# Kernel optimization log

Hardware: AMD Instinct MI355X
Metric: run time of the kernel (lower is better)

Reference implementation:

```python
import jax, jax.numpy as jnp
import numpy as np

VOCAB, EMB, HID = 32000, 32, 256
B, T = 64, 2048


def setup_inputs() -> dict:
    key = jax.random.key(0)
    ks = jax.random.split(key, 7)
    x = jax.random.randint(ks[0], (B, T), 0, VOCAB, dtype=jnp.int64) if jax.config.jax_enable_x64 else jax.random.randint(ks[0], (B, T), 0, VOCAB, dtype=jnp.int32)
    lengths = jax.random.randint(ks[1], (B,), 1, T + 1, dtype=x.dtype)
    emb = jax.random.normal(ks[2], (VOCAB, EMB), dtype=jnp.float32) * 0.02
    emb = emb.at[0].set(0.0)  # padding_idx = 0
    s = 1.0 / np.sqrt(HID)
    W_ih = jax.random.uniform(ks[3], (4 * HID, EMB), jnp.float32, -s, s)
    W_hh = jax.random.uniform(ks[4], (4 * HID, HID), jnp.float32, -s, s)
    b_ih = jax.random.uniform(ks[5], (4 * HID,), jnp.float32, -s, s)
    b_hh = jax.random.uniform(ks[6], (4 * HID,), jnp.float32, -s, s)
    return {"x": x, "lengths": lengths, "emb": emb, "W_ih": W_ih,
            "W_hh": W_hh, "b_ih": b_ih, "b_hh": b_hh}


def _rnn(xe, mask, W_ih, W_hh, b_ih, b_hh):
    # xe: [B, T, EMB]; mask: [B, T] float (1 = valid, 0 = pad)
    Bm, Tm = xe.shape[0], xe.shape[1]
    h0 = jnp.zeros((Bm, HID), xe.dtype)
    c0 = jnp.zeros((Bm, HID), xe.dtype)

    def step(carry, inp):
        h, c = carry
        x_t, m_t = inp  # [B, EMB], [B, 1]
        gates = x_t @ W_ih.T + b_ih + h @ W_hh.T + b_hh  # [B, 4H]
        i, f, g, o = jnp.split(gates, 4, axis=-1)
        i = jax.nn.sigmoid(i)
        f = jax.nn.sigmoid(f)
        g = jnp.tanh(g)
        o = jax.nn.sigmoid(o)
        c_new = f * c + i * g
        h_new = o * jnp.tanh(c_new)
        # masked state update: padded steps keep previous state
        h = m_t * h_new + (1.0 - m_t) * h
        c = m_t * c_new + (1.0 - m_t) * c
        return (h, c), h

    xs = (jnp.swapaxes(xe, 0, 1), jnp.swapaxes(mask, 0, 1)[..., None])
    (_, _), hs = jax.lax.scan(step, (h0, c0), xs)
    return jnp.swapaxes(hs, 0, 1)  # [B, T, HID]


def reference(x, lengths, emb, W_ih, W_hh, b_ih, b_hh):
    xe = emb[x]  # [B, T, EMB]
    mask = (jnp.arange(x.shape[1])[None, :] < lengths[:, None]).astype(xe.dtype)
    out = _rnn(xe, mask, W_ih, W_hh, b_ih, b_hh)  # [B, T, HID]
    last = out[:, -1, :]  # due to mask-freeze, equals state at each length
    return last[:, None, :]  # [B, 1, HID]
```

## Files before the change

kernel.cpp:

```cpp
#include <hip/hip_runtime.h>
#include <hip/hip_fp16.h>

#define EMB 32
#define HID 256
#define BATCH 64
#define TT  2048

typedef _Float16 half8_t __attribute__((ext_vector_type(8)));
typedef _Float16 half2_t __attribute__((ext_vector_type(2)));

#define W_BYTES  (2*36*512*16)
#define BIAS_OFF W_BYTES
#define ACK_OFF  (BIAS_OFF + 4096)
#define FAST_OFF (ACK_OFF + 1024)


__device__ __forceinline__ float fdot2(half2_t a, half2_t b, float c) {
#if __has_builtin(__builtin_amdgcn_fdot2)
    return __builtin_amdgcn_fdot2(a, b, c, false);
#else
    return c + (float)a[0] * (float)b[0] + (float)a[1] * (float)b[1];
#endif
}

__device__ __forceinline__ float dot8(half8_t w, half8_t x, float acc) {
    acc = fdot2(half2_t{w[0], w[1]}, half2_t{x[0], x[1]}, acc);
    acc = fdot2(half2_t{w[2], w[3]}, half2_t{x[2], x[3]}, acc);
    acc = fdot2(half2_t{w[4], w[5]}, half2_t{x[4], x[5]}, acc);
    acc = fdot2(half2_t{w[6], w[7]}, half2_t{x[6], x[7]}, acc);
    return acc;
}

__device__ __forceinline__ float rcp_fast(float v) {
#if __has_builtin(__builtin_amdgcn_rcpf)
    return __builtin_amdgcn_rcpf(v);
#else
    return 1.0f / v;
#endif
}
__device__ __forceinline__ float sigmoid_fast(float v) {
    return rcp_fast(1.0f + __expf(-v));
}
__device__ __forceinline__ float tanh_fast(float v) {
    v = fminf(fmaxf(v, -15.0f), 15.0f);
    float e = __expf(2.0f * v);
    return (e - 1.0f) * rcp_fast(e + 1.0f);
}

__device__ __forceinline__ void barrier_lds() {
    asm volatile("s_waitcnt lgkmcnt(0)\n\ts_barrier" ::: "memory");
}

__device__ __forceinline__ float quad_reduce(float v) {
    int t = __builtin_amdgcn_mov_dpp(__float_as_int(v), 0xB1, 0xF, 0xF, true);
    v += __int_as_float(t);
    t = __builtin_amdgcn_mov_dpp(__float_as_int(v), 0x4E, 0xF, 0xF, true);
    v += __int_as_float(t);
    return v;
}

__device__ __forceinline__ unsigned int load_fast(const unsigned int* p) {
    return *(volatile const unsigned int*)p;
}
__device__ __forceinline__ unsigned int load_slow(const unsigned int* p) {
    return __hip_atomic_load(p, __ATOMIC_RELAXED, __HIP_MEMORY_SCOPE_AGENT);
}

__device__ __forceinline__ int gate_row(int r, int Q) {
    return r == 0 ? Q : r == 1 ? 256 + Q : r == 2 ? 512 + Q : 768 + Q;
}

__global__ void prep_kernel(const float* __restrict__ W_ih,
                            const float* __restrict__ W_hh,
                            const float* __restrict__ b_ih,
                            const float* __restrict__ b_hh,
                            char* __restrict__ ws,
                            unsigned int* __restrict__ outw) {
    int bid = blockIdx.x, t = threadIdx.x;
    if (bid < 72) {
        int R = bid / 36, c = bid % 36;
        int r = c / 9, jj = c % 9;
        int Q = 128 * R + (t >> 2), l = t & 3;
        int row = gate_row(r, Q);
        half8_t v;
#pragma unroll
        for (int e = 0; e < 8; ++e) {
            int p = 8 * jj + e;
            float f;
            if (p < 8)       f = W_ih[row * EMB + 8 * l + p];
            else if (p < 40) f = W_hh[row * HID + 128 * R + 32 * l + (p - 8)];
            else             f = W_hh[row * HID + 128 * (1 - R) + 32 * l + (p - 40)];
            v[e] = (_Float16)f;
        }
        ((half8_t*)ws)[((size_t)bid) * 512 + t] = v;
    } else if (bid == 72) {
        float* bias = (float*)(ws + BIAS_OFF);
        for (int i = t; i < 1024; i += 512) {
            int Q = i >> 2, r = i & 3;
            int row = gate_row(r, Q);
            bias[i] = b_ih[row] + b_hh[row];
        }
    } else if (bid < 105) {
        int g = (bid - 73) * 512 + t;
        outw[g] = ((g >> 6) & 1) ? 0x00010001u : 0u;
    } else {
        int g = (bid - 105) * 512 + t;
        ((unsigned int*)(ws + FAST_OFF))[g] = ((g >> 6) & 1) ? 0x00010001u : 0u;
    }
}

__global__ __launch_bounds__(512, 2) void rnn_kernel(const int* __restrict__ x,
                                                     const int* __restrict__ lengths,
                                                     const float* __restrict__ emb,
                                                     char* __restrict__ ws,
                                                     float* __restrict__ out_) {
    __shared__ __align__(16) _Float16 xhbuf[2][320];

    const int bid  = blockIdx.x;
    const int role = bid >> 6;
    const int b    = bid & 63;
    const int tid  = threadIdx.x;
    const int q    = tid >> 2;
    const int l    = tid & 3;
    const int Q    = 128 * role + q;

    half8_t w[4][9];
    {
        const half8_t* Wp = (const half8_t*)ws + (size_t)role * 36 * 512;
#pragma unroll
        for (int r = 0; r < 4; ++r)
#pragma unroll
            for (int jj = 0; jj < 9; ++jj) w[r][jj] = Wp[(r * 9 + jj) * 512 + tid];
    }
    float4 bs = *(const float4*)(ws + BIAS_OFF + (size_t)Q * 16);

    unsigned int* sexch = (unsigned int*)out_ + (size_t)b * 256;
    unsigned int* fexch = (unsigned int*)(ws + FAST_OFF) + (size_t)b * 256;
    unsigned int* smine = sexch + role * 128;
    unsigned int* spart = sexch + (1 - role) * 128;
    unsigned int* fmine = fexch + role * 128;
    unsigned int* fpart = fexch + (1 - role) * 128;

    int L = lengths[b];
    if (L > TT) L = TT;
    if (L < 1) L = 1;
    const int* __restrict__ xb = x + b * TT;

    if (tid < 320) xhbuf[0][tid] = (_Float16)0.0f;
    __syncthreads();
    if (tid < EMB) {
        float e0 = emb[xb[0] * EMB + tid];
        xhbuf[0][72 * (tid >> 3) + (tid & 7)] = (_Float16)e0;
    }
    __syncthreads();

    float cc = 0.0f, hh = 0.0f;

    float p0 = 0.f, p1 = 0.f, p2 = 0.f, p3 = 0.f;
    {
        const _Float16* cur = xhbuf[0];
        half8_t xv[5];
#pragma unroll
        for (int jj = 0; jj < 5; ++jj) xv[jj] = *(const half8_t*)(cur + 72 * l + 8 * jj);
#pragma unroll
        for (int jj = 0; jj < 5; ++jj) {
            p0 = dot8(w[0][jj], xv[jj], p0);
            p1 = dot8(w[1][jj], xv[jj], p1);
            p2 = dot8(w[2][jj], xv[jj], p2);
            p3 = dot8(w[3][jj], xv[jj], p3);
        }
    }

    int mode = 0;
    int scnt = 0;

#pragma unroll 1
    for (int t = 0; t < L; ++t) {
        const _Float16* __restrict__ cur = xhbuf[t & 1];
        _Float16* __restrict__ nxt = xhbuf[(t + 1) & 1];

        float ev = 0.0f;
        if (tid >= 64 && tid < 64 + EMB) {
            int nt = (t + 1 < L) ? xb[t + 1] : 0;
            ev = emb[nt * EMB + (tid - 64)];
        }

        float a0 = p0, a1 = p1, a2 = p2, a3 = p3;
        {
            half8_t xv[4];
#pragma unroll
            for (int jj = 0; jj < 4; ++jj)
                xv[jj] = *(const half8_t*)(cur + 72 * l + 40 + 8 * jj);
#pragma unroll
            for (int jj = 0; jj < 4; ++jj) {
                a0 = dot8(w[0][5 + jj], xv[jj], a0);
                a1 = dot8(w[1][5 + jj], xv[jj], a1);
                a2 = dot8(w[2][5 + jj], xv[jj], a2);
                a3 = dot8(w[3][5 + jj], xv[jj], a3);
            }
        }

        a0 = quad_reduce(a0);
        a1 = quad_reduce(a1);
        a2 = quad_reduce(a2);
        a3 = quad_reduce(a3);
        float iv = sigmoid_fast(a0 + bs.x);
        float fv = sigmoid_fast(a1 + bs.y);
        float gv = tanh_fast(a2 + bs.z);
        float ov = sigmoid_fast(a3 + bs.w);
        cc = fv * cc + iv * gv;
        hh = ov * tanh_fast(cc);

        const unsigned int tg = ((unsigned)(t + 1) >> 1) & 1u;
        const int ps_ = (t + 1) & 1;

        _Float16 hf = (_Float16)hh;
        unsigned short hb = __builtin_bit_cast(unsigned short, hf);
        unsigned int tb = (unsigned int)((hb & 0xFFFEu) | tg);
        unsigned int nb = (unsigned int)__builtin_amdgcn_mov_dpp((int)tb, 0x104, 0xF, 0xF, true);
        if ((tid & 7) == 0) {
            unsigned int dw = tb | (nb << 16);
            int o = ps_ * 64 + (tid >> 3);
            __hip_atomic_store(fmine + o, dw, __ATOMIC_RELAXED, __HIP_MEMORY_SCOPE_WORKGROUP);
            __hip_atomic_store(smine + o, dw, __ATOMIC_RELAXED, __HIP_MEMORY_SCOPE_AGENT);
        }

        if (l == 0) nxt[72 * (q >> 5) + 8 + (q & 31)] = hf;
        if (tid >= 64 && tid < 64 + EMB) {
            int k = tid - 64;
            nxt[72 * (k >> 3) + (k & 7)] = (_Float16)ev;
        }
        barrier_lds();

        unsigned int fdw = 0;
        const unsigned int* fp = fpart + ps_ * 64 + tid;
        const unsigned int* sp = spart + ps_ * 64 + tid;
        if (tid < 64) fdw = mode ? load_slow(sp) : load_fast(fp);

        p0 = 0.f; p1 = 0.f; p2 = 0.f; p3 = 0.f;
        {
            half8_t xv[5];
#pragma unroll
            for (int jj = 0; jj < 5; ++jj)
                xv[jj] = *(const half8_t*)(nxt + 72 * l + 8 * jj);
#pragma unroll
            for (int jj = 0; jj < 5; ++jj) {
                p0 = dot8(w[0][jj], xv[jj], p0);
                p1 = dot8(w[1][jj], xv[jj], p1);
                p2 = dot8(w[2][jj], xv[jj], p2);
                p3 = dot8(w[3][jj], xv[jj], p3);
            }
        }

        if (tid < 64) {
            unsigned int dw = fdw;
            int tries = 0;
            const int flim = (t == 0) ? 2048 : 24;
            int fell_back = 0;
            while (!__all(((dw & 1u) == tg) && (((dw >> 16) & 1u) == tg))) {
                ++tries;
                if (tries > (1 << 20)) break;
                if (mode || tries > flim) {
                    fell_back = 1;
                    if (tries > flim + 256) __builtin_amdgcn_s_sleep(1);
                    dw = load_slow(sp);
                } else {
                    dw = load_fast(fp);
                }
            }
            if (!mode) {
                scnt = fell_back ? scnt + 1 : 0;
                if (scnt >= 4) mode = 1;
            }
            unsigned short h0 = (unsigned short)(dw & 0xFFFEu);
            unsigned short h1 = (unsigned short)((dw >> 16) & 0xFFFEu);
            int j0 = 2 * tid, j1 = 2 * tid + 1;
            nxt[72 * (j0 >> 5) + 40 + (j0 & 31)] = __builtin_bit_cast(_Float16, h0);
            nxt[72 * (j1 >> 5) + 40 + (j1 & 31)] = __builtin_bit_cast(_Float16, h1);
        }
        barrier_lds();
    }

    int* ack = (int*)(ws + ACK_OFF);
    if (tid == 0)
        __hip_atomic_store(&ack[bid], L, __ATOMIC_RELEASE, __HIP_MEMORY_SCOPE_AGENT);
    if (tid == 0) {
        int tries = 0;
        while (__hip_atomic_load(&ack[bid ^ 64], __ATOMIC_ACQUIRE, __HIP_MEMORY_SCOPE_AGENT) != L) {
            if (++tries > (1 << 20)) break;
            __builtin_amdgcn_s_sleep(8);
        }
    }
    __syncthreads();
    if (l == 0) out_[(size_t)b * 256 + 128 * role + q] = hh;
}

extern "C" void kernel_launch(void* const* d_in, const int* in_sizes, int n_in,
                              void* d_out, int out_size, void* d_ws, size_t ws_size,
                              hipStream_t stream) {
    const int*   x       = (const int*)d_in[0];
    const int*   lengths = (const int*)d_in[1];
    const float* emb     = (const float*)d_in[2];
    const float* W_ih    = (const float*)d_in[3];
    const float* W_hh    = (const float*)d_in[4];
    const float* b_ih    = (const float*)d_in[5];
    const float* b_hh    = (const float*)d_in[6];

    prep_kernel<<<137, 512, 0, stream>>>(W_ih, W_hh, b_ih, b_hh,
                                         (char*)d_ws, (unsigned int*)d_out);
    rnn_kernel<<<128, 512, 0, stream>>>(x, lengths, emb, (char*)d_ws, (float*)d_out);
}
```

Measured before the change: 2.611 ms.

## Pair partner blocks on the same XCD via runtime XCC_ID discovery

Each block reads its hardware XCD id, publishes it to a global table, and after all 128 blocks report, deterministically pairs blocks that share an XCD into the two halves of each batch chain. The per-step hidden-state exchange can then go through the shared L2 of one XCD instead of crossing dies. The fast-path store is also replaced with an inline global_store with sc0. This adds a startup all-block spin on the table, which assumes all 128 blocks are co-resident, and remaps which batch index each pair computes.

Result: faster. 2.515 ms (-3.7%).

```diff
diff --git a/kernel.cpp b/kernel.cpp
--- a/kernel.cpp
+++ b/kernel.cpp
@@ -13,6 +13,7 @@
 #define BIAS_OFF W_BYTES
 #define ACK_OFF  (BIAS_OFF + 4096)
 #define FAST_OFF (ACK_OFF + 1024)
+#define XCD_OFF  (FAST_OFF + 65536)
 
 
 __device__ __forceinline__ float fdot2(half2_t a, half2_t b, float c) {
@@ -61,6 +62,9 @@
 
 __device__ __forceinline__ unsigned int load_fast(const unsigned int* p) {
     return *(volatile const unsigned int*)p;
+}
+__device__ __forceinline__ void store_fast(unsigned int* p, unsigned int v) {
+    asm volatile("global_store_dword %0, %1, off sc0" :: "v"(p), "v"(v) : "memory");
 }
 __device__ __forceinline__ unsigned int load_slow(const unsigned int* p) {
     return __hip_atomic_load(p, __ATOMIC_RELAXED, __HIP_MEMORY_SCOPE_AGENT);
@@ -100,6 +104,8 @@
             int row = gate_row(r, Q);
             bias[i] = b_ih[row] + b_hh[row];
         }
+        if (t < 128)      ((int*)(ws + XCD_OFF))[t] = -1;
+        else if (t < 256) ((int*)(ws + ACK_OFF))[t - 128] = -1;
     } else if (bid < 105) {
         int g = (bid - 73) * 512 + t;
         outw[g] = ((g >> 6) & 1) ? 0x00010001u : 0u;
@@ -115,14 +121,68 @@
                                                      char* __restrict__ ws,
                                                      float* __restrict__ out_) {
     __shared__ __align__(16) _Float16 xhbuf[2][320];
+    __shared__ int sxcd[128];
+    __shared__ int s_chain, s_role, s_partner;
 
     const int bid  = blockIdx.x;
-    const int role = bid >> 6;
-    const int b    = bid & 63;
     const int tid  = threadIdx.x;
     const int q    = tid >> 2;
     const int l    = tid & 3;
-    const int Q    = 128 * role + q;
+
+    {
+        int* xcds = (int*)(ws + XCD_OFF);
+        if (tid == 0) {
+            unsigned int myxcd;
+            asm volatile("s_getreg_b32 %0, hwreg(HW_REG_XCC_ID)" : "=s"(myxcd));
+            __hip_atomic_store(&xcds[bid], (int)(myxcd & 7u),
+                               __ATOMIC_RELEASE, __HIP_MEMORY_SCOPE_AGENT);
+        }
+        if (tid < 128) {
+            int v, tries = 0;
+            do {
+                v = __hip_atomic_load(&xcds[tid], __ATOMIC_ACQUIRE,
+                                      __HIP_MEMORY_SCOPE_AGENT);
+                if (++tries > (1 << 24)) { v = (tid & 7); break; }
+            } while (v < 0);
+            sxcd[tid] = v & 7;
+        }
+        __syncthreads();
+        if (tid == 0) {
+            int pend[8];
+#pragma unroll
+            for (int i = 0; i < 8; ++i) pend[i] = -1;
+            int chain = 0, lone = -1;
+            int mc = -1, mr = 0, mp = bid ^ 64;
+            for (int i = 0; i < 128; ++i) {
+                int xc = sxcd[i];
+                if (pend[xc] < 0) pend[xc] = i;
+                else {
+                    int a = pend[xc]; pend[xc] = -1;
+                    if (a == bid)  { mc = chain; mr = 0; mp = i; }
+                    if (i == bid)  { mc = chain; mr = 1; mp = a; }
+                    ++chain;
+                }
+            }
+            for (int xc = 0; xc < 8; ++xc) {
+                if (pend[xc] < 0) continue;
+                if (lone < 0) lone = pend[xc];
+                else {
+                    int a = lone, bb = pend[xc]; lone = -1;
+                    if (a == bid)  { mc = chain; mr = 0; mp = bb; }
+                    if (bb == bid) { mc = chain; mr = 1; mp = a; }
+                    ++chain;
+                }
+            }
+            if (mc < 0) { mc = bid & 63; mr = bid >> 6; mp = bid ^ 64; }
+            s_chain = mc; s_role = mr; s_partner = mp;
+        }
+        __syncthreads();
+    }
+
+    const int role  = s_role;
+    const int b     = s_chain;
+    const int pbid  = s_partner;
+    const int Q     = 128 * role + q;
 
     half8_t w[4][9];
     {
@@ -219,10 +279,10 @@
         unsigned int tb = (unsigned int)((hb & 0xFFFEu) | tg);
         unsigned int nb = (unsigned int)__builtin_amdgcn_mov_dpp((int)tb, 0x104, 0xF, 0xF, true);
         if ((tid & 7) == 0) {
-            unsigned int dw = tb | (nb << 16);
+            unsigned int dwv = tb | (nb << 16);
             int o = ps_ * 64 + (tid >> 3);
-            __hip_atomic_store(fmine + o, dw, __ATOMIC_RELAXED, __HIP_MEMORY_SCOPE_WORKGROUP);
-            __hip_atomic_store(smine + o, dw, __ATOMIC_RELAXED, __HIP_MEMORY_SCOPE_AGENT);
+            store_fast(fmine + o, dwv);
+            __hip_atomic_store(smine + o, dwv, __ATOMIC_RELAXED, __HIP_MEMORY_SCOPE_AGENT);
         }
 
         if (l == 0) nxt[72 * (q >> 5) + 8 + (q & 31)] = hf;
@@ -286,7 +346,7 @@
         __hip_atomic_store(&ack[bid], L, __ATOMIC_RELEASE, __HIP_MEMORY_SCOPE_AGENT);
     if (tid == 0) {
         int tries = 0;
-        while (__hip_atomic_load(&ack[bid ^ 64], __ATOMIC_ACQUIRE, __HIP_MEMORY_SCOPE_AGENT) != L) {
+        while (__hip_atomic_load(&ack[pbid], __ATOMIC_ACQUIRE, __HIP_MEMORY_SCOPE_AGENT) != L) {
             if (++tries > (1 << 20)) break;
             __builtin_amdgcn_s_sleep(8);
         }
```
